# Kernel tuning notes

Measured on AMD Instinct MI355X. Metric: run time of the kernel, lower is better.

Reference implementation:

```python
import jax, jax.numpy as jnp
import numpy as np

NUM_STUFF = 53
NUM_THING = 80
NUM_CLASSES = NUM_STUFF + NUM_THING  # 133
OBJ_THR = 0.4
OVERLAP_THR = 0.8
B, Q, HM, WM = 2, 100, 160, 160  # mask res = image/4


def setup_inputs() -> dict:
    key = jax.random.key(0)
    k1, k2 = jax.random.split(key)
    # Scale logits so some queries exceed the 0.4 softmax-score threshold.
    logits = 5.0 * jax.random.normal(k1, (B, Q, NUM_CLASSES + 1), dtype=jnp.float32)
    # Give each query a dominant blob (10x10 tile grid) so the greedy
    # overlap-threshold fusion accepts a realistic set of segments.
    th, tw = HM // 10, WM // 10
    tile_id = (jnp.arange(HM) // th)[:, None] * 10 + (jnp.arange(WM) // tw)[None, :]  # [HM,WM]
    bias = jnp.where(tile_id[None, :, :] == jnp.arange(Q)[:, None, None], 8.0, -8.0)  # [Q,HM,WM]
    noise = jax.random.normal(k2, (B, Q, HM, WM), dtype=jnp.float32)
    masks = noise + bias[None]
    return {"logits": logits, "masks": masks, "H": 640, "W": 640}


def reference(logits, masks, H, W):
    """Vectorized, jit-compatible port of Mask2FormerPanoptic._panoptic_merge.

    logits: [B, Q, C+1], masks: [B, Q, h, w]. Returns (sem_seg [B,C,H,W] f32,
    panoptic_seg [B,H,W] int32). The sequential greedy loop is equivalent to a
    per-query acceptance test (areas are loop-invariant) + cumsum id assignment,
    because argmax assigns each pixel to exactly one query.
    """
    Qn = masks.shape[1]

    def merge(lg, mk):
        probs = jax.nn.softmax(lg, axis=-1)               # [Q, C+1]
        scores = jnp.max(probs, axis=-1)                  # [Q]
        labels = jnp.argmax(probs, axis=-1)               # [Q]
        keep = (labels < NUM_CLASSES) & (scores > OBJ_THR)
        # sigmoid then bilinear upsample (half-pixel centers == align_corners=False)
        up = jax.image.resize(jax.nn.sigmoid(mk), (Qn, H, W), method='bilinear')  # [Q,H,W]
        prob_masks = jnp.where(keep[:, None, None], scores[:, None, None] * up, -1.0)
        mask_ids = jnp.argmax(prob_masks, axis=0)         # [H,W]
        mask_area = jnp.zeros((Qn,), jnp.int32).at[mask_ids.ravel()].add(1)  # [Q]
        orig_area = jnp.sum(up >= 0.5, axis=(1, 2))       # [Q]
        accepted = keep & (mask_area > 0) & (orig_area > 0) & (
            mask_area.astype(jnp.float32) > OVERLAP_THR * orig_area.astype(jnp.float32))
        ids = jnp.cumsum(accepted.astype(jnp.int32))      # greedy 1-based segment ids
        panoptic = jnp.where(accepted[mask_ids], ids[mask_ids], 0).astype(jnp.int32)
        masked = jnp.where(accepted[:, None, None], up, 0.0)
        # sem_seg[cls] = max over accepted queries with that class (zeros init)
        sem = jnp.zeros((NUM_CLASSES, H, W), jnp.float32).at[labels].max(masked)
        return sem, panoptic

    return jax.vmap(merge)(logits, masks)
```

## Files before the change

### kernel.cpp

```cpp
#include <hip/hip_runtime.h>
#include <stdint.h>
#include <math.h>

#define NB   2
#define NQ   100
#define NCLS 133
#define NCL1 134
#define HM   160
#define WM   160
#define HO   640
#define WO   640
#define G    8
#define NCELL (HM*WM)

static __device__ __forceinline__ int clampi(int v, int lo, int hi){ return v<lo?lo:(v>hi?hi:v); }
static __device__ __forceinline__ double dsig(float x){ return 1.0/(1.0+exp(-(double)x)); }

__global__ void k_classify(const float* __restrict__ logits, double* __restrict__ scores,
                           int* __restrict__ labels, int* __restrict__ keepf,
                           int* __restrict__ kq, int* __restrict__ Kc,
                           int* __restrict__ marea, int* __restrict__ oarea)
{
  int t = threadIdx.x;
  for (int i=t;i<NB*NQ;i+=blockDim.x){ marea[i]=0; oarea[i]=0; }
  if (t < NB*NQ){
    const float* l = logits + (size_t)t*NCL1;
    float mx = l[0]; int am = 0;
    for (int c=1;c<NCL1;++c){ float v=l[c]; if (v>mx){ mx=v; am=c; } }
    double s = 0.0;
    for (int c=0;c<NCL1;++c) s += exp((double)l[c] - (double)mx);
    double sc = 1.0/s;
    scores[t] = sc; labels[t] = am;
    keepf[t] = (am < NCLS && sc > 0.4) ? 1 : 0;
  }
  __syncthreads();
  if (t < NB){
    int k = 0;
    for (int q=0;q<NQ;++q) if (keepf[t*NQ+q]) kq[t*NQ + (k++)] = q;
    Kc[t] = k;
  }
}

__global__ void k_sigmoid32(const float* __restrict__ masks, float* __restrict__ sig32,
                            const int* __restrict__ keepf)
{
  int gid = blockIdx.x*blockDim.x + threadIdx.x;
  int bq  = gid / (HM*WM/4);
  if (!keepf[bq]) return;
  float4 v = reinterpret_cast<const float4*>(masks)[gid];
  float4 o;
  o.x = (float)dsig(v.x);
  o.y = (float)dsig(v.y);
  o.z = (float)dsig(v.z);
  o.w = (float)dsig(v.w);
  reinterpret_cast<float4*>(sig32)[gid] = o;
}

__global__ __launch_bounds__(256) void k_argmax_part(const float* __restrict__ masks,
        const double* __restrict__ scores, const int* __restrict__ kq,
        const int* __restrict__ Kc, double* __restrict__ pbest, uint8_t* __restrict__ pq,
        int* __restrict__ oarea)
{
  __shared__ double patch[4][6][18];
  __shared__ int oacc[16];
  const int b    = blockIdx.z / G;
  const int g    = blockIdx.z % G;
  const int tid  = threadIdx.x;
  const int lane = tid & 63;
  const int w    = tid >> 6;
  const int tx   = tid & 15, ty = tid >> 4;
  const int wr   = ty & 3;
  const int cj   = blockIdx.x*16 + tx;
  const int ci   = blockIdx.y*16 + ty;
  const int gr0  = blockIdx.y*16 + 4*w - 1;
  const int gc0  = blockIdx.x*16 - 1;
  const int K   = Kc[b];
  const int Kg  = (K + G - 1) / G;
  const int k0  = g*Kg;
  const int k1  = min(K, k0 + Kg);

  if (tid < 16) oacc[tid] = 0;
  __syncthreads();

  double best[4][4];
  int    bq[4][4];
  #pragma unroll
  for (int r=0;r<4;++r)
    #pragma unroll
    for (int s=0;s<4;++s){ best[r][s] = -1.0; bq[r][s] = 0; }

  const int i0 = lane,  p0r = i0/18, p0c = i0-18*p0r;
  const int i1 = lane+64; int p1r = i1/18, p1c = i1-18*p1r;
  const int a0 = clampi(gr0+p0r,0,HM-1)*WM + clampi(gc0+p0c,0,WM-1);
  const int a1 = clampi(gr0+p1r,0,HM-1)*WM + clampi(gc0+p1c,0,WM-1);

  for (int k=k0;k<k1;++k){
    const int    q  = kq[b*NQ+k];
    const double sc = scores[b*NQ+q];
    const float* mp = masks + (size_t)(b*NQ + q)*HM*WM;

    patch[w][p0r][p0c] = dsig(mp[a0]);
    if (lane < 44) patch[w][p1r][p1c] = dsig(mp[a1]);
    asm volatile("" ::: "memory");

    double v[3][3];
    #pragma unroll
    for (int rr=0;rr<3;++rr)
      #pragma unroll
      for (int cc=0;cc<3;++cc)
        v[rr][cc] = patch[w][wr+rr][tx+cc];

    int cnt = 0;
    #pragma unroll
    for (int r=0;r<4;++r){
      const double wa = (r==0)?0.375:(r==1)?0.125:(r==2)?0.875:0.625;
      const double wb = (r==0)?0.625:(r==1)?0.875:(r==2)?0.125:0.375;
      const int ra = (r<2)?0:1, rb = ra+1;
      const bool vedge = (r<2) ? (ci==0) : (ci==HM-1);
      const int  vsel  = (r<2) ? rb : ra;
      double t0 = vedge ? v[vsel][0] : (wa*v[ra][0] + wb*v[rb][0]);
      double t1 = vedge ? v[vsel][1] : (wa*v[ra][1] + wb*v[rb][1]);
      double t2 = vedge ? v[vsel][2] : (wa*v[ra][2] + wb*v[rb][2]);
      double u[4];
      u[0] = (cj==0)    ? t1 : (0.375*t0 + 0.625*t1);
      u[1] = (cj==0)    ? t1 : (0.125*t0 + 0.875*t1);
      u[2] = (cj==WM-1) ? t1 : (0.875*t1 + 0.125*t2);
      u[3] = (cj==WM-1) ? t1 : (0.625*t1 + 0.375*t2);
      #pragma unroll
      for (int s=0;s<4;++s){
        cnt += (u[s] >= 0.5) ? 1 : 0;
        double val = sc*u[s];
        if (val > best[r][s]){ best[r][s] = val; bq[r][s] = q; }
      }
    }
    #pragma unroll
    for (int o2=32;o2>0;o2>>=1) cnt += __shfl_down(cnt, o2);
    if (lane == 0) atomicAdd(&oacc[k-k0], cnt);

    asm volatile("" ::: "memory");
  }

  __syncthreads();
  if (tid < k1-k0){
    int cv = oacc[tid];
    if (cv) atomicAdd(&oarea[b*NQ + kq[b*NQ+k0+tid]], cv);
  }

  const int cell = ci*WM + cj;
  #pragma unroll
  for (int r=0;r<4;++r)
    #pragma unroll
    for (int s=0;s<4;++s){
      size_t idx = ((size_t)((b*G + g)*16 + r*4 + s))*NCELL + cell;
      pbest[idx] = best[r][s];
      pq[idx]    = (uint8_t)bq[r][s];
    }
}

__global__ __launch_bounds__(128) void k_argmax_comb(const double* __restrict__ pbest,
        const uint8_t* __restrict__ pq, uint32_t* __restrict__ mids, int* __restrict__ marea)
{
  __shared__ int hist[NQ];
  const int b   = blockIdx.z;
  const int tid = threadIdx.x;
  const int tx  = tid & 15, ty = tid >> 4;
  const int cj  = blockIdx.x*16 + tx;
  const int ci  = blockIdx.y*8  + ty;
  const int cell= ci*WM + cj;

  for (int i=tid;i<NQ;i+=128) hist[i]=0;
  __syncthreads();

  int bqa[16];
  #pragma unroll
  for (int rs=0;rs<16;++rs){
    double cur = -1.0; int q = 0;
    #pragma unroll
    for (int g2=0;g2<G;++g2){
      size_t idx = ((size_t)((b*G + g2)*16 + rs))*NCELL + cell;
      double v = pbest[idx];
      if (v > cur){ cur = v; q = (int)pq[idx]; }
    }
    bqa[rs] = q;
  }

  #pragma unroll
  for (int r=0;r<4;++r){
    uint32_t w = (uint32_t)bqa[r*4+0] | ((uint32_t)bqa[r*4+1]<<8)
               | ((uint32_t)bqa[r*4+2]<<16) | ((uint32_t)bqa[r*4+3]<<24);
    int y = 4*ci + r;
    mids[(b*HO + y)*(WO/4) + cj] = w;
  }
  #pragma unroll
  for (int rs=0;rs<16;++rs)
    atomicAdd(&hist[bqa[rs]], 1);
  __syncthreads();
  for (int i=tid;i<NQ;i+=128)
    if (hist[i]) atomicAdd(&marea[b*NQ+i], hist[i]);
}

__global__ void k_finalize(const int* __restrict__ keepf, const int* __restrict__ labels,
                           const int* __restrict__ marea, const int* __restrict__ oarea,
                           float* __restrict__ fid, int* __restrict__ chanoff,
                           int* __restrict__ sortedq)
{
  const int b = blockIdx.x;
  const int tid = threadIdx.x;
  __shared__ int acc[NQ], lab[NQ], cntS[NCLS], start[NCLS];
  if (tid < NQ){
    int i = b*NQ + tid;
    int ma = marea[i], oa = oarea[i];
    acc[tid] = (keepf[i] && ma>0 && oa>0 && ((double)ma > 0.8*(double)oa)) ? 1 : 0;
    lab[tid] = labels[i];
  }
  if (tid < NCLS) cntS[tid]=0;
  __syncthreads();
  if (tid == 0){
    int A = 0;
    for (int q=0;q<NQ;++q){
      if (acc[q]){ A++; fid[b*NQ+q] = (float)A; cntS[lab[q]]++; }
      else fid[b*NQ+q] = 0.0f;
    }
    int off = 0;
    for (int c=0;c<NCLS;++c){ start[c]=off; chanoff[b*NCL1+c]=off; off += cntS[c]; }
    chanoff[b*NCL1+NCLS] = off;
    for (int q=0;q<NQ;++q)
      if (acc[q]){ int c=lab[q]; sortedq[b*NQ + start[c]] = q; start[c]++; }
  }
}

__global__ void k_pan(const uint32_t* __restrict__ mids, const float* __restrict__ fid,
                      float* __restrict__ out)
{
  int t = blockIdx.x*blockDim.x + threadIdx.x;
  int b = t / (HO*WO/4);
  uint32_t w = mids[t];
  float4 o;
  o.x = fid[b*NQ + (w & 255u)];
  o.y = fid[b*NQ + ((w>>8) & 255u)];
  o.z = fid[b*NQ + ((w>>16) & 255u)];
  o.w = fid[b*NQ + (w>>24)];
  reinterpret_cast<float4*>(out)[(size_t)NB*NCLS*(HO*(size_t)WO/4) + t] = o;
}

__global__ __launch_bounds__(256) void k_sem(const float* __restrict__ sig32,
        const int* __restrict__ chanoff, const int* __restrict__ sortedq,
        float* __restrict__ out)
{
  const int bc = blockIdx.z;
  const int b  = bc / NCLS, c = bc - b*NCLS;
  const int tid = threadIdx.x;
  const int tx  = tid & 15, ty = tid >> 4;
  const int cj  = blockIdx.x*16 + tx;
  const int ci  = blockIdx.y*16 + ty;
  const int s0 = chanoff[b*NCL1+c], s1 = chanoff[b*NCL1+c+1];

  float acc[4][4];
  #pragma unroll
  for (int r=0;r<4;++r)
    #pragma unroll
    for (int s=0;s<4;++s) acc[r][s]=0.f;

  if (s1 > s0){
    const int rm = max(ci-1,0), rp = min(ci+1,HM-1);
    const int cm = max(cj-1,0), cp = min(cj+1,WM-1);
    for (int i=s0;i<s1;++i){
      const int q = sortedq[b*NQ+i];
      const float* sp = sig32 + (size_t)(b*NQ+q)*HM*WM;
      float v[3][3];
      v[0][0]=sp[rm*WM+cm]; v[0][1]=sp[rm*WM+cj]; v[0][2]=sp[rm*WM+cp];
      v[1][0]=sp[ci*WM+cm]; v[1][1]=sp[ci*WM+cj]; v[1][2]=sp[ci*WM+cp];
      v[2][0]=sp[rp*WM+cm]; v[2][1]=sp[rp*WM+cj]; v[2][2]=sp[rp*WM+cp];
      #pragma unroll
      for (int r=0;r<4;++r){
        const float wa = (r==0)?0.375f:(r==1)?0.125f:(r==2)?0.875f:0.625f;
        const float wb = (r==0)?0.625f:(r==1)?0.875f:(r==2)?0.125f:0.375f;
        const int ra = (r<2)?0:1, rb = ra+1;
        const bool vedge = (r<2) ? (ci==0) : (ci==HM-1);
        const int  vsel  = (r<2) ? rb : ra;
        float t0 = vedge ? v[vsel][0] : (wa*v[ra][0] + wb*v[rb][0]);
        float t1 = vedge ? v[vsel][1] : (wa*v[ra][1] + wb*v[rb][1]);
        float t2 = vedge ? v[vsel][2] : (wa*v[ra][2] + wb*v[rb][2]);
        float u0 = (cj==0)    ? t1 : (0.375f*t0 + 0.625f*t1);
        float u1 = (cj==0)    ? t1 : (0.125f*t0 + 0.875f*t1);
        float u2 = (cj==WM-1) ? t1 : (0.875f*t1 + 0.125f*t2);
        float u3 = (cj==WM-1) ? t1 : (0.625f*t1 + 0.375f*t2);
        acc[r][0] = fmaxf(acc[r][0], u0);
        acc[r][1] = fmaxf(acc[r][1], u1);
        acc[r][2] = fmaxf(acc[r][2], u2);
        acc[r][3] = fmaxf(acc[r][3], u3);
      }
    }
  }
  #pragma unroll
  for (int r=0;r<4;++r){
    float4 o; o.x=acc[r][0]; o.y=acc[r][1]; o.z=acc[r][2]; o.w=acc[r][3];
    reinterpret_cast<float4*>(out)[((size_t)bc*HO + (4*ci+r))*(WO/4) + cj] = o;
  }
}

extern "C" void kernel_launch(void* const* d_in, const int* in_sizes, int n_in,
                              void* d_out, int out_size, void* d_ws, size_t ws_size,
                              hipStream_t stream)
{
  const float* logits = (const float*)d_in[0];
  const float* masks  = (const float*)d_in[1];
  float* out = (float*)d_out;

  char* ws = (char*)d_ws;
  size_t off = 0;
  auto alloc = [&](size_t bytes)->void*{
    void* p = ws + off; off = (off + bytes + 255) & ~(size_t)255; return p;
  };
  float*    sig32   = (float*)   alloc((size_t)NB*NQ*HM*WM*sizeof(float));
  double*   pbest   = (double*)  alloc((size_t)NB*G*16*NCELL*sizeof(double));
  uint8_t*  pq      = (uint8_t*) alloc((size_t)NB*G*16*NCELL*sizeof(uint8_t));
  uint32_t* mids    = (uint32_t*)alloc((size_t)NB*HO*(WO/4)*sizeof(uint32_t));
  double*   scores  = (double*)  alloc(NB*NQ*sizeof(double));
  int*      labels  = (int*)     alloc(NB*NQ*sizeof(int));
  int*      keepf   = (int*)     alloc(NB*NQ*sizeof(int));
  int*      kq      = (int*)     alloc(NB*NQ*sizeof(int));
  int*      Kc      = (int*)     alloc(NB*sizeof(int));
  int*      marea   = (int*)     alloc(NB*NQ*sizeof(int));
  int*      oarea   = (int*)     alloc(NB*NQ*sizeof(int));
  float*    fid     = (float*)   alloc(NB*NQ*sizeof(float));
  int*      chanoff = (int*)     alloc(NB*NCL1*sizeof(int));
  int*      sortedq = (int*)     alloc(NB*NQ*sizeof(int));

  hipLaunchKernelGGL(k_classify, dim3(1), dim3(256), 0, stream,
                     logits, scores, labels, keepf, kq, Kc, marea, oarea);
  hipLaunchKernelGGL(k_sigmoid32, dim3((NB*NQ*HM*WM/4)/256), dim3(256), 0, stream,
                     masks, sig32, keepf);
  hipLaunchKernelGGL(k_argmax_part, dim3(WM/16, HM/16, NB*G), dim3(256), 0, stream,
                     masks, scores, kq, Kc, pbest, pq, oarea);
  hipLaunchKernelGGL(k_argmax_comb, dim3(WM/16, HM/8, NB), dim3(128), 0, stream,
                     pbest, pq, mids, marea);
  hipLaunchKernelGGL(k_finalize, dim3(NB), dim3(192), 0, stream,
                     keepf, labels, marea, oarea, fid, chanoff, sortedq);
  hipLaunchKernelGGL(k_pan, dim3((NB*HO*WO/4)/256), dim3(256), 0, stream,
                     mids, fid, out);
  hipLaunchKernelGGL(k_sem, dim3(WM/16, HM/16, NB*NCLS), dim3(256), 0, stream,
                     sig32, chanoff, sortedq, out);
}
```

Measured before the change: 260.2 us.

## Precompute f64 sigmoid, pack argmax score+index, row-tile semantic kernel

The sigmoid kernel now writes both double and float sigmoid maps, so the argmax kernel reads precomputed doubles instead of recomputing exp per block. Per-group partial argmax results pack the score and query index into a single 64-bit word, so the combine is an integer max over one array. The semantic-map kernel is reorganized into full-width row tiles, with input rows staged in shared memory and fully contiguous output writes. This adds an extra double buffer in memory, and truncating low mantissa bits may alter near-tie resolution.

After: 228.0 us. 12.4% less time.

```diff
diff --git a/kernel.cpp b/kernel.cpp
--- a/kernel.cpp
+++ b/kernel.cpp
@@ -12,6 +12,7 @@
 #define WO   640
 #define G    8
 #define NCELL (HM*WM)
+#define SEMROWS 16
 
 static __device__ __forceinline__ int clampi(int v, int lo, int hi){ return v<lo?lo:(v>hi?hi:v); }
 static __device__ __forceinline__ double dsig(float x){ return 1.0/(1.0+exp(-(double)x)); }
@@ -41,24 +42,25 @@
   }
 }
 
-__global__ void k_sigmoid32(const float* __restrict__ masks, float* __restrict__ sig32,
-                            const int* __restrict__ keepf)
+__global__ void k_sigmoid(const float* __restrict__ masks, double* __restrict__ sig64,
+                          float* __restrict__ sig32, const int* __restrict__ keepf)
 {
   int gid = blockIdx.x*blockDim.x + threadIdx.x;
   int bq  = gid / (HM*WM/4);
   if (!keepf[bq]) return;
   float4 v = reinterpret_cast<const float4*>(masks)[gid];
-  float4 o;
-  o.x = (float)dsig(v.x);
-  o.y = (float)dsig(v.y);
-  o.z = (float)dsig(v.z);
-  o.w = (float)dsig(v.w);
-  reinterpret_cast<float4*>(sig32)[gid] = o;
-}
-
-__global__ __launch_bounds__(256) void k_argmax_part(const float* __restrict__ masks,
+  double o0 = dsig(v.x), o1 = dsig(v.y), o2 = dsig(v.z), o3 = dsig(v.w);
+  double2 d0; d0.x=o0; d0.y=o1;
+  double2 d1; d1.x=o2; d1.y=o3;
+  reinterpret_cast<double2*>(sig64)[gid*2]   = d0;
+  reinterpret_cast<double2*>(sig64)[gid*2+1] = d1;
+  float4 f; f.x=(float)o0; f.y=(float)o1; f.z=(float)o2; f.w=(float)o3;
+  reinterpret_cast<float4*>(sig32)[gid] = f;
+}
+
+__global__ __launch_bounds__(256) void k_argmax_part(const double* __restrict__ sig64,
         const double* __restrict__ scores, const int* __restrict__ kq,
-        const int* __restrict__ Kc, double* __restrict__ pbest, uint8_t* __restrict__ pq,
+        const int* __restrict__ Kc, unsigned long long* __restrict__ ppack,
         int* __restrict__ oarea)
 {
   __shared__ double patch[4][6][18];
@@ -97,10 +99,10 @@
   for (int k=k0;k<k1;++k){
     const int    q  = kq[b*NQ+k];
     const double sc = scores[b*NQ+q];
-    const float* mp = masks + (size_t)(b*NQ + q)*HM*WM;
-
-    patch[w][p0r][p0c] = dsig(mp[a0]);
-    if (lane < 44) patch[w][p1r][p1c] = dsig(mp[a1]);
+    const double* sp = sig64 + (size_t)(b*NQ + q)*HM*WM;
+
+    patch[w][p0r][p0c] = sp[a0];
+    if (lane < 44) patch[w][p1r][p1c] = sp[a1];
     asm volatile("" ::: "memory");
 
     double v[3][3];
@@ -151,14 +153,22 @@
   for (int r=0;r<4;++r)
     #pragma unroll
     for (int s=0;s<4;++s){
+      unsigned long long pk = 0ULL;
+      if (k0 < k1)
+        pk = ((unsigned long long)__double_as_longlong(best[r][s]) & ~127ULL)
+           | (unsigned long long)(127 - bq[r][s]);
       size_t idx = ((size_t)((b*G + g)*16 + r*4 + s))*NCELL + cell;
-      pbest[idx] = best[r][s];
-      pq[idx]    = (uint8_t)bq[r][s];
-    }
-}
-
-__global__ __launch_bounds__(128) void k_argmax_comb(const double* __restrict__ pbest,
-        const uint8_t* __restrict__ pq, uint32_t* __restrict__ mids, int* __restrict__ marea)
+      ppack[idx] = pk;
+    }
+}
+
+static __device__ __forceinline__ int decode_q(unsigned long long v){
+  int q = 127 - (int)(v & 127ULL);
+  return clampi(q, 0, NQ-1);
+}
+
+__global__ __launch_bounds__(128) void k_argmax_comb(const unsigned long long* __restrict__ ppack,
+        uint32_t* __restrict__ mids, int* __restrict__ marea)
 {
   __shared__ int hist[NQ];
   const int b   = blockIdx.z;
@@ -174,14 +184,13 @@
   int bqa[16];
   #pragma unroll
   for (int rs=0;rs<16;++rs){
-    double cur = -1.0; int q = 0;
+    unsigned long long cur = 0ULL;
     #pragma unroll
     for (int g2=0;g2<G;++g2){
-      size_t idx = ((size_t)((b*G + g2)*16 + rs))*NCELL + cell;
-      double v = pbest[idx];
-      if (v > cur){ cur = v; q = (int)pq[idx]; }
-    }
-    bqa[rs] = q;
+      unsigned long long v = ppack[((size_t)((b*G + g2)*16 + rs))*NCELL + cell];
+      if (v > cur) cur = v;
+    }
+    bqa[rs] = decode_q(cur);
   }
 
   #pragma unroll
@@ -247,56 +256,63 @@
         const int* __restrict__ chanoff, const int* __restrict__ sortedq,
         float* __restrict__ out)
 {
-  const int bc = blockIdx.z;
+  const int bc = blockIdx.y;
   const int b  = bc / NCLS, c = bc - b*NCLS;
+  const int y0 = blockIdx.x * SEMROWS;
+  const int ci0 = y0 >> 2;
   const int tid = threadIdx.x;
-  const int tx  = tid & 15, ty = tid >> 4;
-  const int cj  = blockIdx.x*16 + tx;
-  const int ci  = blockIdx.y*16 + ty;
   const int s0 = chanoff[b*NCL1+c], s1 = chanoff[b*NCL1+c+1];
 
-  float acc[4][4];
-  #pragma unroll
-  for (int r=0;r<4;++r)
-    #pragma unroll
-    for (int s=0;s<4;++s) acc[r][s]=0.f;
-
-  if (s1 > s0){
-    const int rm = max(ci-1,0), rp = min(ci+1,HM-1);
-    const int cm = max(cj-1,0), cp = min(cj+1,WM-1);
-    for (int i=s0;i<s1;++i){
-      const int q = sortedq[b*NQ+i];
-      const float* sp = sig32 + (size_t)(b*NQ+q)*HM*WM;
-      float v[3][3];
-      v[0][0]=sp[rm*WM+cm]; v[0][1]=sp[rm*WM+cj]; v[0][2]=sp[rm*WM+cp];
-      v[1][0]=sp[ci*WM+cm]; v[1][1]=sp[ci*WM+cj]; v[1][2]=sp[ci*WM+cp];
-      v[2][0]=sp[rp*WM+cm]; v[2][1]=sp[rp*WM+cj]; v[2][2]=sp[rp*WM+cp];
-      #pragma unroll
-      for (int r=0;r<4;++r){
-        const float wa = (r==0)?0.375f:(r==1)?0.125f:(r==2)?0.875f:0.625f;
-        const float wb = (r==0)?0.625f:(r==1)?0.875f:(r==2)?0.125f:0.375f;
-        const int ra = (r<2)?0:1, rb = ra+1;
-        const bool vedge = (r<2) ? (ci==0) : (ci==HM-1);
-        const int  vsel  = (r<2) ? rb : ra;
-        float t0 = vedge ? v[vsel][0] : (wa*v[ra][0] + wb*v[rb][0]);
-        float t1 = vedge ? v[vsel][1] : (wa*v[ra][1] + wb*v[rb][1]);
-        float t2 = vedge ? v[vsel][2] : (wa*v[ra][2] + wb*v[rb][2]);
-        float u0 = (cj==0)    ? t1 : (0.375f*t0 + 0.625f*t1);
-        float u1 = (cj==0)    ? t1 : (0.125f*t0 + 0.875f*t1);
-        float u2 = (cj==WM-1) ? t1 : (0.875f*t1 + 0.125f*t2);
-        float u3 = (cj==WM-1) ? t1 : (0.625f*t1 + 0.375f*t2);
-        acc[r][0] = fmaxf(acc[r][0], u0);
-        acc[r][1] = fmaxf(acc[r][1], u1);
-        acc[r][2] = fmaxf(acc[r][2], u2);
-        acc[r][3] = fmaxf(acc[r][3], u3);
-      }
-    }
-  }
-  #pragma unroll
-  for (int r=0;r<4;++r){
-    float4 o; o.x=acc[r][0]; o.y=acc[r][1]; o.z=acc[r][2]; o.w=acc[r][3];
-    reinterpret_cast<float4*>(out)[((size_t)bc*HO + (4*ci+r))*(WO/4) + cj] = o;
-  }
+  __shared__ float row[6][WM];
+
+  float4 acc[10];
+  #pragma unroll
+  for (int ch=0;ch<10;++ch) acc[ch] = make_float4(0.f,0.f,0.f,0.f);
+
+  for (int i=s0;i<s1;++i){
+    const int q = sortedq[b*NQ+i];
+    const float* sp = sig32 + (size_t)(b*NQ+q)*HM*WM;
+    for (int i2=tid;i2<6*WM;i2+=256){
+      int jr = i2/WM, jc = i2 - jr*WM;
+      int gi = clampi(ci0 + jr - 1, 0, HM-1);
+      row[jr][jc] = sp[gi*WM + jc];
+    }
+    __syncthreads();
+    #pragma unroll
+    for (int ch=0;ch<10;++ch){
+      const int idx = ch*256 + tid;
+      const int yo  = idx / WM;
+      const int x4  = idx - yo*WM;
+      const int y   = y0 + yo;
+      const int ci  = y >> 2, r = y & 3;
+      const int ciL = ci - ci0 + 1;
+      const int ra  = (r<2) ? ciL-1 : ciL;
+      const int rb  = ra + 1;
+      const bool vedge = (r<2) ? (ci==0) : (ci==HM-1);
+      const int cm = max(x4-1,0), cp = min(x4+1,WM-1);
+      const float wa = (r==0)?0.375f:(r==1)?0.125f:(r==2)?0.875f:0.625f;
+      const float wb = (r==0)?0.625f:(r==1)?0.875f:(r==2)?0.125f:0.375f;
+      float am=row[ra][cm], a0=row[ra][x4], ap=row[ra][cp];
+      float bm=row[rb][cm], b0=row[rb][x4], bp=row[rb][cp];
+      float t0 = vedge ? ((r<2) ? bm : am) : (wa*am + wb*bm);
+      float t1 = vedge ? ((r<2) ? b0 : a0) : (wa*a0 + wb*b0);
+      float t2 = vedge ? ((r<2) ? bp : ap) : (wa*ap + wb*bp);
+      float u0 = (x4==0)    ? t1 : (0.375f*t0 + 0.625f*t1);
+      float u1 = (x4==0)    ? t1 : (0.125f*t0 + 0.875f*t1);
+      float u2 = (x4==WM-1) ? t1 : (0.875f*t1 + 0.125f*t2);
+      float u3 = (x4==WM-1) ? t1 : (0.625f*t1 + 0.375f*t2);
+      acc[ch].x = fmaxf(acc[ch].x, u0);
+      acc[ch].y = fmaxf(acc[ch].y, u1);
+      acc[ch].z = fmaxf(acc[ch].z, u2);
+      acc[ch].w = fmaxf(acc[ch].w, u3);
+    }
+    __syncthreads();
+  }
+
+  float4* ob = reinterpret_cast<float4*>(out) + ((size_t)bc*HO + y0)*(WO/4);
+  #pragma unroll
+  for (int ch=0;ch<10;++ch)
+    ob[ch*256 + tid] = acc[ch];
 }
 
 extern "C" void kernel_launch(void* const* d_in, const int* in_sizes, int n_in,
@@ -312,9 +328,10 @@
   auto alloc = [&](size_t bytes)->void*{
     void* p = ws + off; off = (off + bytes + 255) & ~(size_t)255; return p;
   };
+  double*   sig64   = (double*)  alloc((size_t)NB*NQ*HM*WM*sizeof(double));
   float*    sig32   = (float*)   alloc((size_t)NB*NQ*HM*WM*sizeof(float));
-  double*   pbest   = (double*)  alloc((size_t)NB*G*16*NCELL*sizeof(double));
-  uint8_t*  pq      = (uint8_t*) alloc((size_t)NB*G*16*NCELL*sizeof(uint8_t));
+  unsigned long long* ppack = (unsigned long long*)
+                               alloc((size_t)NB*G*16*NCELL*sizeof(unsigned long long));
   uint32_t* mids    = (uint32_t*)alloc((size_t)NB*HO*(WO/4)*sizeof(uint32_t));
   double*   scores  = (double*)  alloc(NB*NQ*sizeof(double));
   int*      labels  = (int*)     alloc(NB*NQ*sizeof(int));
@@ -329,16 +346,16 @@
 
   hipLaunchKernelGGL(k_classify, dim3(1), dim3(256), 0, stream,
                      logits, scores, labels, keepf, kq, Kc, marea, oarea);
-  hipLaunchKernelGGL(k_sigmoid32, dim3((NB*NQ*HM*WM/4)/256), dim3(256), 0, stream,
-                     masks, sig32, keepf);
+  hipLaunchKernelGGL(k_sigmoid, dim3((NB*NQ*HM*WM/4)/256), dim3(256), 0, stream,
+                     masks, sig64, sig32, keepf);
   hipLaunchKernelGGL(k_argmax_part, dim3(WM/16, HM/16, NB*G), dim3(256), 0, stream,
-                     masks, scores, kq, Kc, pbest, pq, oarea);
+                     sig64, scores, kq, Kc, ppack, oarea);
   hipLaunchKernelGGL(k_argmax_comb, dim3(WM/16, HM/8, NB), dim3(128), 0, stream,
-                     pbest, pq, mids, marea);
+                     ppack, mids, marea);
   hipLaunchKernelGGL(k_finalize, dim3(NB), dim3(192), 0, stream,
                      keepf, labels, marea, oarea, fid, chanoff, sortedq);
   hipLaunchKernelGGL(k_pan, dim3((NB*HO*WO/4)/256), dim3(256), 0, stream,
                      mids, fid, out);
-  hipLaunchKernelGGL(k_sem, dim3(WM/16, HM/16, NB*NCLS), dim3(256), 0, stream,
+  hipLaunchKernelGGL(k_sem, dim3(HO/SEMROWS, NB*NCLS), dim3(256), 0, stream,
                      sig32, chanoff, sortedq, out);
 }
```
